# Performance work log

Hardware: AMD Instinct MI355X
Metric: run time of the kernel (lower is better)

The kernel has to match this reference:

```python
import jax, jax.numpy as jnp
import numpy as np

NQ = 8          # n_qubits (attention and ffn)
DIM = 2 ** NQ   # state-vector dimension
EPS = 1e-5      # nn.LayerNorm default eps


def _layernorm(x, g, b):
    m = jnp.mean(x, axis=-1, keepdims=True)
    v = jnp.mean((x - m) ** 2, axis=-1, keepdims=True)
    return (x - m) * jax.lax.rsqrt(v + EPS) * g + b


def _attn_quantum(tok, theta):
    """Batched 8-qubit state-vector sim: RX(tok_i)+RX(theta_i) per wire, CNOT ring, <Z_i>.
    tok: [N, 8] -> returns [N, 8]."""
    N = tok.shape[0]
    half = 0.5 * (tok + theta)  # RX(a)RX(b) = RX(a+b) on same wire
    # per-wire amplitude RX(a)|0> = (cos(a/2), -i sin(a/2))
    re = jnp.stack([jnp.cos(half), jnp.zeros_like(half)], axis=-1)
    im = jnp.stack([jnp.zeros_like(half), -jnp.sin(half)], axis=-1)
    amp = jax.lax.complex(re, im)  # [N, 8, 2]
    # build product state with wire 0 as the leading qubit axis: [N, 2, ..., 2]
    state = amp[:, 0, :]
    for w in range(1, NQ):
        state = state[..., None] * amp[:, w, :].reshape((N,) + (1,) * w + (2,))
    # CNOT ring: (0,1),(1,2),...,(6,7),(7,0)
    pairs = [(i, i + 1) for i in range(NQ - 1)] + [(NQ - 1, 0)]
    for c, t in pairs:
        flipped = jnp.flip(state, axis=t + 1)
        mask = jnp.arange(2).reshape((1,) * (c + 1) + (2,) + (1,) * (NQ - 1 - c))
        state = jnp.where(mask == 1, flipped, state)
    probs = (state.real ** 2 + state.imag ** 2).reshape(N, DIM)
    # <Z_w> = sum_k probs[k] * (1 - 2*bit_w(k)); wire 0 is most significant bit
    bits = (jnp.arange(DIM)[None, :] >> (NQ - 1 - jnp.arange(NQ)[:, None])) & 1
    signs = (1.0 - 2.0 * bits).astype(probs.dtype)  # [8, 256]
    return probs @ signs.T


def _ffn_quantum(tok, phi):
    """Product state per wire: RY(phi_i) RX(tok_i) |0>, then <Z_i>. tok: [..., 8]."""
    ct, st = jnp.cos(0.5 * tok), jnp.sin(0.5 * tok)
    cp, sp = jnp.cos(0.5 * phi), jnp.sin(0.5 * phi)
    # v0 = cp*ct + i*sp*st ; v1 = sp*ct - i*cp*st ; z = |v0|^2 - |v1|^2
    return (cp * ct) ** 2 + (sp * st) ** 2 - (sp * ct) ** 2 - (cp * st) ** 2


def setup_inputs() -> dict:
    key = jax.random.key(0)
    ks = jax.random.split(key, 8)
    B, S, E, F = 32, 2048, 8, 2048
    x = jax.random.normal(ks[0], (B, S, E), dtype=jnp.float32)
    theta = jax.random.uniform(ks[1], (NQ,), dtype=jnp.float32, minval=-np.pi, maxval=np.pi)
    phi = jax.random.uniform(ks[2], (NQ,), dtype=jnp.float32, minval=-np.pi, maxval=np.pi)
    W1 = jax.random.normal(ks[3], (F, NQ), dtype=jnp.float32) / np.sqrt(NQ)
    b1 = jax.random.normal(ks[4], (F,), dtype=jnp.float32) * 0.01
    W2 = jax.random.normal(ks[5], (E, F), dtype=jnp.float32) / np.sqrt(F)
    b2 = jax.random.normal(ks[6], (E,), dtype=jnp.float32) * 0.01
    gamma1 = jnp.ones((E,), dtype=jnp.float32)
    beta1 = jnp.zeros((E,), dtype=jnp.float32)
    gamma2 = jnp.ones((E,), dtype=jnp.float32)
    beta2 = jnp.zeros((E,), dtype=jnp.float32)
    return {"x": x, "theta": theta, "phi": phi, "W1": W1, "b1": b1, "W2": W2,
            "b2": b2, "gamma1": gamma1, "beta1": beta1, "gamma2": gamma2, "beta2": beta2}


def reference(x, theta, phi, W1, b1, W2, b2, gamma1, beta1, gamma2, beta2):
    B, S, E = x.shape
    attn = _attn_quantum(x.reshape(B * S, E), theta).reshape(B, S, E)
    h = _layernorm(x + attn, gamma1, beta1)            # dropout is identity (eval)
    z = _ffn_quantum(h, phi)                            # [B, S, 8]
    f = jax.nn.relu(z @ W1.T + b1) @ W2.T + b2          # linear1 -> relu -> linear2
    return _layernorm(h + f, gamma2, beta2)
```

## Files before the change

kernel.cpp:

```cpp
#include <hip/hip_runtime.h>
#include <math.h>

#define NQ 8
#define FDIM 2048
#define EPSV 1e-5f

typedef __attribute__((ext_vector_type(8))) short short8v;
typedef __attribute__((ext_vector_type(16))) float f32x16;

__device__ __forceinline__ unsigned pk_bf16(float lo, float hi) {
    unsigned r;
    asm("v_cvt_pk_bf16_f32 %0, %1, %2" : "=v"(r) : "v"(lo), "v"(hi));
    return r;
}

__device__ __forceinline__ short8v pack4(unsigned a, unsigned b, unsigned c, unsigned d) {
    uint4 w; w.x = a; w.y = b; w.z = c; w.w = d;
    return __builtin_bit_cast(short8v, w);
}

#define MFMA32 __builtin_amdgcn_mfma_f32_32x32x16_bf16

#define RP(C, d0, d1)                                                   \
  d0 = pack4(pk_bf16(fmaxf(C[0], 0.f),  fmaxf(C[1], 0.f)),              \
             pk_bf16(fmaxf(C[2], 0.f),  fmaxf(C[3], 0.f)),              \
             pk_bf16(fmaxf(C[4], 0.f),  fmaxf(C[5], 0.f)),              \
             pk_bf16(fmaxf(C[6], 0.f),  fmaxf(C[7], 0.f)));             \
  d1 = pack4(pk_bf16(fmaxf(C[8], 0.f),  fmaxf(C[9], 0.f)),              \
             pk_bf16(fmaxf(C[10], 0.f), fmaxf(C[11], 0.f)),             \
             pk_bf16(fmaxf(C[12], 0.f), fmaxf(C[13], 0.f)),             \
             pk_bf16(fmaxf(C[14], 0.f), fmaxf(C[15], 0.f)))

#define ITER(AUSE, ALOAD, B0USE, B1USE, C2IDX)                          \
  {                                                                     \
    short8v p00, p01, p10, p11;                                         \
    RP(C1_0, p00, p01); RP(C1_1, p10, p11);                             \
    C1_0 = MFMA32(AUSE, b1S0, zeroC, 0, 0, 0);                          \
    C1_1 = MFMA32(AUSE, b1S1, zeroC, 0, 0, 0);                          \
    acc0 = MFMA32(p00, B0USE, acc0, 0, 0, 0);                           \
    acc1 = MFMA32(p10, B0USE, acc1, 0, 0, 0);                           \
    acc0 = MFMA32(p01, B1USE, acc0, 0, 0, 0);                           \
    acc1 = MFMA32(p11, B1USE, acc1, 0, 0, 0);                           \
    short8v p20, p21, p30, p31;                                         \
    RP(C1_2, p20, p21); RP(C1_3, p30, p31);                             \
    C1_2 = MFMA32(AUSE, b1S2, zeroC, 0, 0, 0);                          \
    C1_3 = MFMA32(AUSE, b1S3, zeroC, 0, 0, 0);                          \
    acc2 = MFMA32(p20, B0USE, acc2, 0, 0, 0);                           \
    acc3 = MFMA32(p30, B0USE, acc3, 0, 0, 0);                           \
    acc2 = MFMA32(p21, B1USE, acc2, 0, 0, 0);                           \
    acc3 = MFMA32(p31, B1USE, acc3, 0, 0, 0);                           \
    ALOAD = *reinterpret_cast<const short8v*>(W1p + (C2IDX) * 512);     \
    B0USE = *reinterpret_cast<const short8v*>(W2p + (C2IDX) * 32);      \
    B1USE = *reinterpret_cast<const short8v*>(W2p + (C2IDX) * 32 + 16); \
  }

__launch_bounds__(512, 2)
__global__ void qtb_kernel(const float* __restrict__ x,
                           const float* __restrict__ theta,
                           const float* __restrict__ phi,
                           const float* __restrict__ W1,
                           const float* __restrict__ b1,
                           const float* __restrict__ W2,
                           const float* __restrict__ b2,
                           const float* __restrict__ g1,
                           const float* __restrict__ be1,
                           const float* __restrict__ g2,
                           const float* __restrict__ be2,
                           float* __restrict__ out)
{
    __shared__ short W1f[64 * 512];
    __shared__ short W2s[8 * 2056];
    __shared__ float park[8][1024];
    __shared__ float hLds[256 * 8];

    const int tid = threadIdx.x;

    for (int k = tid; k < FDIM; k += 512) {
        const float4 wa = *reinterpret_cast<const float4*>(W1 + (size_t)k * NQ);
        const float4 wb = *reinterpret_cast<const float4*>(W1 + (size_t)k * NQ + 4);
        const float bk = b1[k];
        unsigned* d0 = reinterpret_cast<unsigned*>(&W1f[(k >> 5) * 512 + (k & 31) * 8]);
        unsigned* d1 = reinterpret_cast<unsigned*>(&W1f[(k >> 5) * 512 + ((k & 31) + 32) * 8]);
        d0[0] = pk_bf16(wa.x, wa.y); d0[1] = pk_bf16(wa.z, wa.w);
        d0[2] = pk_bf16(bk, 0.f);    d0[3] = 0u;
        d1[0] = pk_bf16(wb.x, wb.y); d1[1] = pk_bf16(wb.z, wb.w);
        d1[2] = 0u;                  d1[3] = 0u;
    }
    for (int idx = tid; idx < 8 * 512; idx += 512) {
        const int i = idx >> 9, kq = idx & 511;
        const int k0 = kq * 4;
        const float4 w = *reinterpret_cast<const float4*>(W2 + (size_t)i * FDIM + k0);
        const int quad = (k0 >> 2) & 3;
        const int posq = (0x3120 >> (quad * 4)) & 0xF;
        const int dcol = (k0 & ~15) | (posq * 4);
        uint2 pkw; pkw.x = pk_bf16(w.x, w.y); pkw.y = pk_bf16(w.z, w.w);
        *reinterpret_cast<uint2*>(&W2s[i * 2056 + dcol]) = pkw;
    }
    __syncthreads();

    const int lane = tid & 63;
    const int wid  = tid >> 6;
    const int g    = wid & 1;
    const int q    = wid >> 1;
    const int hi2  = lane >> 5;
    const int il   = lane & 31;
    const int tbase = blockIdx.x * 256 + g * 128;

    float h[2][8];
    unsigned zpkt[2][4];
#pragma unroll
    for (int tt = 0; tt < 2; ++tt) {
        const int token = tbase + tt * 64 + lane;
        const float4 xa = reinterpret_cast<const float4*>(x + (size_t)token * NQ)[0];
        const float4 xb = reinterpret_cast<const float4*>(x + (size_t)token * NQ)[1];
        const float xv[8] = {xa.x, xa.y, xa.z, xa.w, xb.x, xb.y, xb.z, xb.w};

        float c[8];
#pragma unroll
        for (int j = 0; j < 8; ++j) c[j] = __cosf(xv[j] + theta[j]);
        float attn[8];
        attn[0] = ((c[1] * c[2]) * (c[3] * c[4])) * ((c[5] * c[6]) * c[7]);
        {
            float p = c[0];
#pragma unroll
            for (int j = 1; j < 8; ++j) { p *= c[j]; attn[j] = p; }
        }
        float s[8];
#pragma unroll
        for (int j = 0; j < 8; ++j) s[j] = xv[j] + attn[j];
        float mean = 0.f;
#pragma unroll
        for (int j = 0; j < 8; ++j) mean += s[j];
        mean *= 0.125f;
        float var = 0.f;
#pragma unroll
        for (int j = 0; j < 8; ++j) { float d = s[j] - mean; var = fmaf(d, d, var); }
        var *= 0.125f;
        const float rs = rsqrtf(var + EPSV);
#pragma unroll
        for (int j = 0; j < 8; ++j) h[tt][j] = (s[j] - mean) * rs * g1[j] + be1[j];

        float zv[8];
#pragma unroll
        for (int j = 0; j < 8; ++j) zv[j] = __cosf(phi[j]) * __cosf(h[tt][j]);
#pragma unroll
        for (int p = 0; p < 4; ++p) zpkt[tt][p] = pk_bf16(zv[2 * p], zv[2 * p + 1]);
    }

    if (q == 0) {
        float4* hp0 = reinterpret_cast<float4*>(&hLds[(g * 128 + lane) * 8]);
        hp0[0] = make_float4(h[0][0], h[0][1], h[0][2], h[0][3]);
        hp0[1] = make_float4(h[0][4], h[0][5], h[0][6], h[0][7]);
        float4* hp1 = reinterpret_cast<float4*>(&hLds[(g * 128 + 64 + lane) * 8]);
        hp1[0] = make_float4(h[1][0], h[1][1], h[1][2], h[1][3]);
        hp1[1] = make_float4(h[1][4], h[1][5], h[1][6], h[1][7]);
    }

    unsigned zs[2][2][4];
#pragma unroll
    for (int tt = 0; tt < 2; ++tt)
#pragma unroll
        for (int p = 0; p < 4; ++p) {
            zs[tt][0][p] = (unsigned)__shfl((int)zpkt[tt][p], il);
            zs[tt][1][p] = (unsigned)__shfl((int)zpkt[tt][p], 32 + il);
        }
    const unsigned biasv = 0x00003f80u;
    const short8v b1S0 = pack4(hi2 ? zs[0][0][2] : zs[0][0][0],
                               hi2 ? zs[0][0][3] : zs[0][0][1],
                               hi2 ? 0u : biasv, 0u);
    const short8v b1S1 = pack4(hi2 ? zs[0][1][2] : zs[0][1][0],
                               hi2 ? zs[0][1][3] : zs[0][1][1],
                               hi2 ? 0u : biasv, 0u);
    const short8v b1S2 = pack4(hi2 ? zs[1][0][2] : zs[1][0][0],
                               hi2 ? zs[1][0][3] : zs[1][0][1],
                               hi2 ? 0u : biasv, 0u);
    const short8v b1S3 = pack4(hi2 ? zs[1][1][2] : zs[1][1][0],
                               hi2 ? zs[1][1][3] : zs[1][1][1],
                               hi2 ? 0u : biasv, 0u);

    f32x16 zeroC;
#pragma unroll
    for (int e = 0; e < 16; ++e) zeroC[e] = 0.f;
    f32x16 acc0 = zeroC, acc1 = zeroC, acc2 = zeroC, acc3 = zeroC;

    const int ir = il & 7;
    const int lo = q * 16;

    const short* W1p = &W1f[lane * 8];
    const short* W2p = &W2s[ir * 2056 + hi2 * 8];

    short8v A1a = *reinterpret_cast<const short8v*>(W1p + lo * 512);
    short8v B0a = *reinterpret_cast<const short8v*>(W2p + lo * 32);
    short8v B1a = *reinterpret_cast<const short8v*>(W2p + lo * 32 + 16);
    f32x16 C1_0 = MFMA32(A1a, b1S0, zeroC, 0, 0, 0);
    f32x16 C1_1 = MFMA32(A1a, b1S1, zeroC, 0, 0, 0);
    f32x16 C1_2 = MFMA32(A1a, b1S2, zeroC, 0, 0, 0);
    f32x16 C1_3 = MFMA32(A1a, b1S3, zeroC, 0, 0, 0);
    short8v A1b = *reinterpret_cast<const short8v*>(W1p + (lo + 1) * 512);
    short8v B0b = *reinterpret_cast<const short8v*>(W2p + (lo + 1) * 32);
    short8v B1b = *reinterpret_cast<const short8v*>(W2p + (lo + 1) * 32 + 16);

#pragma unroll 1
    for (int t = 0; t < 16; t += 2) {
        ITER(A1b, A1a, B0a, B1a, lo + ((t + 2) & 15));
        ITER(A1a, A1b, B0b, B1b, lo + ((t + 3) & 15));
    }

    if (il < 8) {
        float* fb = &park[wid][0];
#pragma unroll
        for (int r = 0; r < 16; ++r) {
            const int trow = (r & 3) + 8 * (r >> 2) + 4 * hi2;
            fb[trow * 8 + il]         = acc0[r];
            fb[(32 + trow) * 8 + il]  = acc1[r];
            fb[(64 + trow) * 8 + il]  = acc2[r];
            fb[(96 + trow) * 8 + il]  = acc3[r];
        }
    }
    __syncthreads();

    if (q == 0) {
#pragma unroll
        for (int tt = 0; tt < 2; ++tt) {
            const int tloc = tt * 64 + lane;
            float fv[8] = {0.f, 0.f, 0.f, 0.f, 0.f, 0.f, 0.f, 0.f};
#pragma unroll
            for (int qq = 0; qq < 4; ++qq) {
                const float* pb = &park[qq * 2 + g][tloc * 8];
                const float4 f0 = *reinterpret_cast<const float4*>(pb);
                const float4 f1 = *reinterpret_cast<const float4*>(pb + 4);
                fv[0] += f0.x; fv[1] += f0.y; fv[2] += f0.z; fv[3] += f0.w;
                fv[4] += f1.x; fv[5] += f1.y; fv[6] += f1.z; fv[7] += f1.w;
            }

            const float4 h0 = reinterpret_cast<const float4*>(&hLds[(g * 128 + tloc) * 8])[0];
            const float4 h1 = reinterpret_cast<const float4*>(&hLds[(g * 128 + tloc) * 8])[1];
            const float hv[8] = {h0.x, h0.y, h0.z, h0.w, h1.x, h1.y, h1.z, h1.w};

            float y[8];
#pragma unroll
            for (int j = 0; j < 8; ++j) y[j] = hv[j] + fv[j] + b2[j];
            float mean2 = 0.f;
#pragma unroll
            for (int j = 0; j < 8; ++j) mean2 += y[j];
            mean2 *= 0.125f;
            float var2 = 0.f;
#pragma unroll
            for (int j = 0; j < 8; ++j) { float d = y[j] - mean2; var2 = fmaf(d, d, var2); }
            var2 *= 0.125f;
            const float rs2 = rsqrtf(var2 + EPSV);

            float o[8];
#pragma unroll
            for (int j = 0; j < 8; ++j) o[j] = (y[j] - mean2) * rs2 * g2[j] + be2[j];

            const int token = blockIdx.x * 256 + g * 128 + tloc;
            float4* op = reinterpret_cast<float4*>(out + (size_t)token * NQ);
            op[0] = make_float4(o[0], o[1], o[2], o[3]);
            op[1] = make_float4(o[4], o[5], o[6], o[7]);
        }
    }
}

extern "C" void kernel_launch(void* const* d_in, const int* in_sizes, int n_in,
                              void* d_out, int out_size, void* d_ws, size_t ws_size,
                              hipStream_t stream) {
    const float* x     = (const float*)d_in[0];
    const float* theta = (const float*)d_in[1];
    const float* phi   = (const float*)d_in[2];
    const float* W1    = (const float*)d_in[3];
    const float* b1    = (const float*)d_in[4];
    const float* W2    = (const float*)d_in[5];
    const float* b2    = (const float*)d_in[6];
    const float* g1    = (const float*)d_in[7];
    const float* be1   = (const float*)d_in[8];
    const float* g2    = (const float*)d_in[9];
    const float* be2   = (const float*)d_in[10];
    float* out = (float*)d_out;

    const int ntok = in_sizes[0] / NQ;
    const int grid = ntok / 256;

    qtb_kernel<<<grid, 512, 0, stream>>>(x, theta, phi, W1, b1, W2, b2,
                                         g1, be1, g2, be2, out);
}
```

Before: 22.47 us.

## Overlap weight staging loads with token prologue and fully unroll MFMA loop

```diff
diff --git a/kernel.cpp b/kernel.cpp
--- a/kernel.cpp
+++ b/kernel.cpp
@@ -22,14 +22,11 @@
 #define MFMA32 __builtin_amdgcn_mfma_f32_32x32x16_bf16
 
 #define RP(C, d0, d1)                                                   \
-  d0 = pack4(pk_bf16(fmaxf(C[0], 0.f),  fmaxf(C[1], 0.f)),              \
-             pk_bf16(fmaxf(C[2], 0.f),  fmaxf(C[3], 0.f)),              \
-             pk_bf16(fmaxf(C[4], 0.f),  fmaxf(C[5], 0.f)),              \
-             pk_bf16(fmaxf(C[6], 0.f),  fmaxf(C[7], 0.f)));             \
-  d1 = pack4(pk_bf16(fmaxf(C[8], 0.f),  fmaxf(C[9], 0.f)),              \
-             pk_bf16(fmaxf(C[10], 0.f), fmaxf(C[11], 0.f)),             \
-             pk_bf16(fmaxf(C[12], 0.f), fmaxf(C[13], 0.f)),             \
-             pk_bf16(fmaxf(C[14], 0.f), fmaxf(C[15], 0.f)))
+  { const f32x16 m_ = __builtin_elementwise_max(C, zeroC);              \
+    d0 = pack4(pk_bf16(m_[0],  m_[1]),  pk_bf16(m_[2],  m_[3]),         \
+               pk_bf16(m_[4],  m_[5]),  pk_bf16(m_[6],  m_[7]));        \
+    d1 = pack4(pk_bf16(m_[8],  m_[9]),  pk_bf16(m_[10], m_[11]),        \
+               pk_bf16(m_[12], m_[13]), pk_bf16(m_[14], m_[15])); }
 
 #define ITER(AUSE, ALOAD, B0USE, B1USE, C2IDX)                          \
   {                                                                     \
@@ -73,31 +70,7 @@
     __shared__ float park[8][1024];
     __shared__ float hLds[256 * 8];
 
-    const int tid = threadIdx.x;
-
-    for (int k = tid; k < FDIM; k += 512) {
-        const float4 wa = *reinterpret_cast<const float4*>(W1 + (size_t)k * NQ);
-        const float4 wb = *reinterpret_cast<const float4*>(W1 + (size_t)k * NQ + 4);
-        const float bk = b1[k];
-        unsigned* d0 = reinterpret_cast<unsigned*>(&W1f[(k >> 5) * 512 + (k & 31) * 8]);
-        unsigned* d1 = reinterpret_cast<unsigned*>(&W1f[(k >> 5) * 512 + ((k & 31) + 32) * 8]);
-        d0[0] = pk_bf16(wa.x, wa.y); d0[1] = pk_bf16(wa.z, wa.w);
-        d0[2] = pk_bf16(bk, 0.f);    d0[3] = 0u;
-        d1[0] = pk_bf16(wb.x, wb.y); d1[1] = pk_bf16(wb.z, wb.w);
-        d1[2] = 0u;                  d1[3] = 0u;
-    }
-    for (int idx = tid; idx < 8 * 512; idx += 512) {
-        const int i = idx >> 9, kq = idx & 511;
-        const int k0 = kq * 4;
-        const float4 w = *reinterpret_cast<const float4*>(W2 + (size_t)i * FDIM + k0);
-        const int quad = (k0 >> 2) & 3;
-        const int posq = (0x3120 >> (quad * 4)) & 0xF;
-        const int dcol = (k0 & ~15) | (posq * 4);
-        uint2 pkw; pkw.x = pk_bf16(w.x, w.y); pkw.y = pk_bf16(w.z, w.w);
-        *reinterpret_cast<uint2*>(&W2s[i * 2056 + dcol]) = pkw;
-    }
-    __syncthreads();
-
+    const int tid  = threadIdx.x;
     const int lane = tid & 63;
     const int wid  = tid >> 6;
     const int g    = wid & 1;
@@ -106,14 +79,34 @@
     const int il   = lane & 31;
     const int tbase = blockIdx.x * 256 + g * 128;
 
+    const float4 xA0 = reinterpret_cast<const float4*>(x + (size_t)(tbase + lane) * NQ)[0];
+    const float4 xA1 = reinterpret_cast<const float4*>(x + (size_t)(tbase + lane) * NQ)[1];
+    const float4 xB0 = reinterpret_cast<const float4*>(x + (size_t)(tbase + 64 + lane) * NQ)[0];
+    const float4 xB1 = reinterpret_cast<const float4*>(x + (size_t)(tbase + 64 + lane) * NQ)[1];
+
+    float4 w1lo[4], w1hi[4]; float bk4[4];
+#pragma unroll
+    for (int it = 0; it < 4; ++it) {
+        const int k = tid + it * 512;
+        w1lo[it] = *reinterpret_cast<const float4*>(W1 + (size_t)k * NQ);
+        w1hi[it] = *reinterpret_cast<const float4*>(W1 + (size_t)k * NQ + 4);
+        bk4[it]  = b1[k];
+    }
+    float4 w2v[8];
+#pragma unroll
+    for (int it = 0; it < 8; ++it) {
+        const int idx = tid + it * 512;
+        const int i = idx >> 9, kq = idx & 511;
+        w2v[it] = *reinterpret_cast<const float4*>(W2 + (size_t)i * FDIM + kq * 4);
+    }
+
     float h[2][8];
     unsigned zpkt[2][4];
 #pragma unroll
     for (int tt = 0; tt < 2; ++tt) {
-        const int token = tbase + tt * 64 + lane;
-        const float4 xa = reinterpret_cast<const float4*>(x + (size_t)token * NQ)[0];
-        const float4 xb = reinterpret_cast<const float4*>(x + (size_t)token * NQ)[1];
-        const float xv[8] = {xa.x, xa.y, xa.z, xa.w, xb.x, xb.y, xb.z, xb.w};
+        const float4 x0 = tt ? xB0 : xA0;
+        const float4 x1 = tt ? xB1 : xA1;
+        const float xv[8] = {x0.x, x0.y, x0.z, x0.w, x1.x, x1.y, x1.z, x1.w};
 
         float c[8];
 #pragma unroll
@@ -178,32 +171,54 @@
                                hi2 ? zs[1][1][3] : zs[1][1][1],
                                hi2 ? 0u : biasv, 0u);
 
+#pragma unroll
+    for (int it = 0; it < 4; ++it) {
+        const int k = tid + it * 512;
+        uint4 d0, d1;
+        d0.x = pk_bf16(w1lo[it].x, w1lo[it].y); d0.y = pk_bf16(w1lo[it].z, w1lo[it].w);
+        d0.z = pk_bf16(bk4[it], 0.f);           d0.w = 0u;
+        d1.x = pk_bf16(w1hi[it].x, w1hi[it].y); d1.y = pk_bf16(w1hi[it].z, w1hi[it].w);
+        d1.z = 0u;                              d1.w = 0u;
+        *reinterpret_cast<uint4*>(&W1f[(k >> 5) * 512 + (k & 31) * 8])        = d0;
+        *reinterpret_cast<uint4*>(&W1f[(k >> 5) * 512 + ((k & 31) + 32) * 8]) = d1;
+    }
+#pragma unroll
+    for (int it = 0; it < 8; ++it) {
+        const int idx = tid + it * 512;
+        const int i = idx >> 9, kq = idx & 511;
+        const int k0 = kq * 4;
+        const int quad = (k0 >> 2) & 3;
+        const int posq = (0x3120 >> (quad * 4)) & 0xF;
+        const int dcol = (k0 & ~15) | (posq * 4);
+        uint2 pkw; pkw.x = pk_bf16(w2v[it].x, w2v[it].y); pkw.y = pk_bf16(w2v[it].z, w2v[it].w);
+        *reinterpret_cast<uint2*>(&W2s[i * 2056 + dcol]) = pkw;
+    }
+    __syncthreads();
+
     f32x16 zeroC;
 #pragma unroll
     for (int e = 0; e < 16; ++e) zeroC[e] = 0.f;
     f32x16 acc0 = zeroC, acc1 = zeroC, acc2 = zeroC, acc3 = zeroC;
 
     const int ir = il & 7;
-    const int lo = q * 16;
-
-    const short* W1p = &W1f[lane * 8];
-    const short* W2p = &W2s[ir * 2056 + hi2 * 8];
-
-    short8v A1a = *reinterpret_cast<const short8v*>(W1p + lo * 512);
-    short8v B0a = *reinterpret_cast<const short8v*>(W2p + lo * 32);
-    short8v B1a = *reinterpret_cast<const short8v*>(W2p + lo * 32 + 16);
+    const short* W1p = &W1f[(q * 16) * 512 + lane * 8];
+    const short* W2p = &W2s[ir * 2056 + (q * 16) * 32 + hi2 * 8];
+
+    short8v A1a = *reinterpret_cast<const short8v*>(W1p);
+    short8v B0a = *reinterpret_cast<const short8v*>(W2p);
+    short8v B1a = *reinterpret_cast<const short8v*>(W2p + 16);
     f32x16 C1_0 = MFMA32(A1a, b1S0, zeroC, 0, 0, 0);
     f32x16 C1_1 = MFMA32(A1a, b1S1, zeroC, 0, 0, 0);
     f32x16 C1_2 = MFMA32(A1a, b1S2, zeroC, 0, 0, 0);
     f32x16 C1_3 = MFMA32(A1a, b1S3, zeroC, 0, 0, 0);
-    short8v A1b = *reinterpret_cast<const short8v*>(W1p + (lo + 1) * 512);
-    short8v B0b = *reinterpret_cast<const short8v*>(W2p + (lo + 1) * 32);
-    short8v B1b = *reinterpret_cast<const short8v*>(W2p + (lo + 1) * 32 + 16);
-
-#pragma unroll 1
+    short8v A1b = *reinterpret_cast<const short8v*>(W1p + 512);
+    short8v B0b = *reinterpret_cast<const short8v*>(W2p + 32);
+    short8v B1b = *reinterpret_cast<const short8v*>(W2p + 32 + 16);
+
+#pragma unroll
     for (int t = 0; t < 16; t += 2) {
-        ITER(A1b, A1a, B0a, B1a, lo + ((t + 2) & 15));
-        ITER(A1a, A1b, B0b, B1b, lo + ((t + 3) & 15));
+        ITER(A1b, A1a, B0a, B1a, (t + 2) & 15);
+        ITER(A1a, A1b, B0b, B1b, (t + 3) & 15);
     }
 
     if (il < 8) {
```

Measured after the change: 20.56 us. -8.5%, faster.
